# Optimization experiments

Hardware: AMD Instinct MI355X
Metric: run time of the kernel (lower is better)

Reference implementation:

```python
import jax, jax.numpy as jnp
import numpy as np

B, G, D, H, W = 2, 8, 32, 128, 160
NEIGH = 9           # evaluate_neighbors
PROP = 1            # propagation_out_range - 1
PAD1 = int(np.sqrt(NEIGH) / 2) + PROP      # = 2
PAD2 = PAD1 * 2                            # = 4


def setup_inputs() -> dict:
    key = jax.random.key(0)
    ks = jax.random.split(key, 8)
    x1 = jax.random.normal(ks[0], (B, G, D, H, W), jnp.float32)
    offset = jax.random.uniform(ks[1], (B, 2 * NEIGH, H, W), jnp.float32)
    weight = jax.random.uniform(ks[2], (B, 1, H, W), jnp.float32)
    # 1x1x1 Conv3d weights stored as [out_ch, in_ch]; BN folded to scale/bias (eval mode)
    w0 = jax.random.normal(ks[3], (16, G), jnp.float32) * 0.1
    bn0_scale = jnp.ones((16,), jnp.float32)
    bn0_bias = jnp.zeros((16,), jnp.float32)
    w1 = jax.random.normal(ks[4], (8, 16), jnp.float32) * 0.1
    bn1_scale = jnp.ones((8,), jnp.float32)
    bn1_bias = jnp.zeros((8,), jnp.float32)
    w_sim = jax.random.normal(ks[5], (1, 8), jnp.float32) * 0.1
    b_sim = jnp.zeros((1,), jnp.float32)
    return {"x1": x1, "offset": offset, "weight": weight,
            "w0": w0, "bn0_scale": bn0_scale, "bn0_bias": bn0_bias,
            "w1": w1, "bn1_scale": bn1_scale, "bn1_bias": bn1_bias,
            "w_sim": w_sim, "b_sim": b_sim}


def _conv1x1_bn_relu(x, w, scale, bias):
    # x: [B,Cin,D,H,W], w: [Cout,Cin]
    y = jnp.einsum('bcdhw,oc->bodhw', x, w)
    return jax.nn.relu(y * scale[None, :, None, None, None] + bias[None, :, None, None, None])


def reference(x1, offset, weight, w0, bn0_scale, bn0_bias, w1, bn1_scale, bn1_bias, w_sim, b_sim):
    h = _conv1x1_bn_relu(x1, w0, bn0_scale, bn0_bias)          # [B,16,D,H,W]
    h = _conv1x1_bn_relu(h, w1, bn1_scale, bn1_bias)            # [B,8,D,H,W]
    sim = jnp.einsum('bcdhw,oc->bodhw', h, w_sim) + b_sim[None, :, None, None, None]
    sim = sim[:, 0]                                             # [B,D,H,W]
    b, d, hgt, wid = sim.shape
    p1 = jnp.pad(sim, ((0, 0), (0, 0), (PAD1, PAD1), (PAD1, PAD1)), mode='reflect')
    p2 = jnp.pad(sim, ((0, 0), (0, 0), (PAD2, PAD2), (PAD2, PAD2)), mode='reflect')
    side = int(np.sqrt(NEIGH))  # 3
    acc = jnp.zeros_like(sim)
    for s in range(NEIGH):
        iy, ix = s // side, s % side
        # wide-dilation crop (stride (PROP+1)*2 = 4) over the double-padded map
        c2 = p2[:, :, iy * 4: iy * 4 + hgt, ix * 4: ix * 4 + wid]
        # narrow-dilation crop (stride PROP+1 = 2) over the single-padded map
        c1 = p1[:, :, iy * 2: iy * 2 + hgt, ix * 2: ix * 2 + wid]
        w_wide = offset[:, s][:, None]            # [B,1,H,W] -> broadcast over depth
        w_narrow = offset[:, s + NEIGH][:, None]
        acc = acc + (w_narrow * c1 + w_wide * c2) * 0.5
    return acc * weight                                          # weight [B,1,H,W]
```

## Files before the change

### kernel.cpp

```cpp
#include <hip/hip_runtime.h>

#define Bc 2
#define Gc 8
#define Dc 32
#define Hc 128
#define Wc 160
#define HW (Hc * Wc)
#define DHW (Dc * HW)

#define TH 32
#define TW 40
#define R  4
#define SH (TH + 2 * R)
#define SW (TW + 2 * R)
#define SIMN (SH * SW)
#define NQ (SIMN / 4)
#define QPR (SW / 4)
#define NQ2 (TH * TW / 4)
#define QPR2 (TW / 4)

__global__ __launch_bounds__(512)
void fused_kernel(
    const float* __restrict__ x1, const float* __restrict__ offset,
    const float* __restrict__ weight,
    const float* __restrict__ w0, const float* __restrict__ s0, const float* __restrict__ b0,
    const float* __restrict__ w1, const float* __restrict__ s1, const float* __restrict__ b1,
    const float* __restrict__ wsim, const float* __restrict__ bsim,
    float* __restrict__ out)
{
    __shared__ __align__(16) float sms[SIMN];
    __shared__ float smw[289];
    const int tid = threadIdx.x;

    if (tid < 289) {
        const int i = tid;
        float v;
        if (i < 128)      v = w0[i] * s0[i >> 3];
        else if (i < 144) v = b0[i - 128];
        else if (i < 272) v = w1[i - 144] * s1[(i - 144) >> 4];
        else if (i < 280) v = b1[i - 272];
        else if (i < 288) v = wsim[i - 280];
        else              v = bsim[0];
        smw[i] = v;
    }

    const int blk = blockIdx.x;
    const int d   = blk & 31;
    const int t   = (blk >> 5) & 15;
    const int b   = blk >> 9;
    const int h0t = (t >> 2) * TH;
    const int w0t = (t & 3) * TW;

    __syncthreads();

    const float* sw0 = smw;
    const float* sb0 = smw + 128;
    const float* sw1 = smw + 144;
    const float* sb1 = smw + 272;
    const float* sws = smw + 280;
    const float  sbs = smw[288];

    const float* xb = x1 + (size_t)b * (Gc * DHW) + (size_t)d * HW;

    if (tid < NQ) {
        const int q   = tid;
        const int ty  = q / QPR;
        const int tx0 = (q - ty * QPR) * 4;
        int gh = h0t - R + ty;
        gh = gh < 0 ? -gh : (gh >= Hc ? 2 * Hc - 2 - gh : gh);
        const int gw0 = w0t - R + tx0;

        float4 xv[Gc];
        if (gw0 >= 0 && gw0 <= Wc - 4) {
            const float* p = xb + gh * Wc + gw0;
#pragma unroll
            for (int g = 0; g < Gc; ++g)
                xv[g] = *reinterpret_cast<const float4*>(p + g * DHW);
        } else {
            int gw[4];
#pragma unroll
            for (int j = 0; j < 4; ++j) {
                int x = gw0 + j;
                gw[j] = x < 0 ? -x : (x >= Wc ? 2 * Wc - 2 - x : x);
            }
            const float* p = xb + gh * Wc;
#pragma unroll
            for (int g = 0; g < Gc; ++g) {
                xv[g].x = p[g * DHW + gw[0]];
                xv[g].y = p[g * DHW + gw[1]];
                xv[g].z = p[g * DHW + gw[2]];
                xv[g].w = p[g * DHW + gw[3]];
            }
        }

        float4 acc1[8];
#pragma unroll
        for (int c = 0; c < 8; ++c) {
            const float bb = sb1[c];
            acc1[c].x = bb; acc1[c].y = bb; acc1[c].z = bb; acc1[c].w = bb;
        }

#pragma unroll
        for (int o = 0; o < 16; ++o) {
            float ax = sb0[o], ay = ax, az = ax, aw = ax;
#pragma unroll
            for (int g = 0; g < Gc; ++g) {
                const float wv = sw0[o * Gc + g];
                ax = fmaf(wv, xv[g].x, ax);
                ay = fmaf(wv, xv[g].y, ay);
                az = fmaf(wv, xv[g].z, az);
                aw = fmaf(wv, xv[g].w, aw);
            }
            ax = fmaxf(ax, 0.f);
            ay = fmaxf(ay, 0.f);
            az = fmaxf(az, 0.f);
            aw = fmaxf(aw, 0.f);
#pragma unroll
            for (int c = 0; c < 8; ++c) {
                const float wv = sw1[c * 16 + o];
                acc1[c].x = fmaf(wv, ax, acc1[c].x);
                acc1[c].y = fmaf(wv, ay, acc1[c].y);
                acc1[c].z = fmaf(wv, az, acc1[c].z);
                acc1[c].w = fmaf(wv, aw, acc1[c].w);
            }
        }

        float sx = sbs, sy = sbs, sz = sbs, sw = sbs;
#pragma unroll
        for (int c = 0; c < 8; ++c) {
            const float ws = sws[c];
            sx = fmaf(ws, fmaxf(acc1[c].x, 0.f), sx);
            sy = fmaf(ws, fmaxf(acc1[c].y, 0.f), sy);
            sz = fmaf(ws, fmaxf(acc1[c].z, 0.f), sz);
            sw = fmaf(ws, fmaxf(acc1[c].w, 0.f), sw);
        }

        float4 r; r.x = sx; r.y = sy; r.z = sz; r.w = sw;
        *reinterpret_cast<float4*>(&sms[q * 4]) = r;
    }

    __builtin_amdgcn_sched_barrier(0);

    const int oy  = tid / QPR2;
    const int ox  = (tid - oy * QPR2) * 4;
    const int hw4 = (h0t + oy) * Wc + (w0t + ox);

    float4 off4[18];
    float4 wt4;
    if (tid < NQ2) {
        const float* offb = offset + (size_t)b * 18 * HW;
#pragma unroll
        for (int s = 0; s < 18; ++s)
            off4[s] = *reinterpret_cast<const float4*>(offb + s * HW + hw4);
        wt4 = *reinterpret_cast<const float4*>(weight + (size_t)b * HW + hw4);
    }

    __syncthreads();

    if (tid < NQ2) {
        const float* sp = sms + (oy + R) * SW + (ox + R);
        float ax = 0.f, ay = 0.f, az = 0.f, aw = 0.f;
#pragma unroll
        for (int s = 0; s < 9; ++s) {
            const int dy = s / 3 - 1, dx = s % 3 - 1;
            const float4 cw = *reinterpret_cast<const float4*>(sp + dy * 4 * SW + dx * 4);
            const float* np = sp + dy * 2 * SW + dx * 2;
            const float2 n0 = *reinterpret_cast<const float2*>(np);
            const float2 n1 = *reinterpret_cast<const float2*>(np + 2);
            const float4 ow = off4[s];
            const float4 on = off4[s + 9];
            ax = fmaf(on.x, n0.x, fmaf(ow.x, cw.x, ax));
            ay = fmaf(on.y, n0.y, fmaf(ow.y, cw.y, ay));
            az = fmaf(on.z, n1.x, fmaf(ow.z, cw.z, az));
            aw = fmaf(on.w, n1.y, fmaf(ow.w, cw.w, aw));
        }
        float4 r;
        r.x = ax * 0.5f * wt4.x;
        r.y = ay * 0.5f * wt4.y;
        r.z = az * 0.5f * wt4.z;
        r.w = aw * 0.5f * wt4.w;
        float* outb = out + (size_t)(b * Dc + d) * HW;
        *reinterpret_cast<float4*>(outb + hw4) = r;
    }
}

extern "C" void kernel_launch(void* const* d_in, const int* in_sizes, int n_in,
                              void* d_out, int out_size, void* d_ws, size_t ws_size,
                              hipStream_t stream)
{
    const float* x1     = (const float*)d_in[0];
    const float* offset = (const float*)d_in[1];
    const float* weight = (const float*)d_in[2];
    const float* w0     = (const float*)d_in[3];
    const float* s0     = (const float*)d_in[4];
    const float* b0     = (const float*)d_in[5];
    const float* w1     = (const float*)d_in[6];
    const float* s1     = (const float*)d_in[7];
    const float* b1     = (const float*)d_in[8];
    const float* wsim   = (const float*)d_in[9];
    const float* bsim   = (const float*)d_in[10];
    float* out = (float*)d_out;

    fused_kernel<<<1024, 512, 0, stream>>>(x1, offset, weight,
                                           w0, s0, b0, w1, s1, b1, wsim, bsim,
                                           out);
}
```

Measured before the change: 120.0 us.

## Split fused kernel into separate MLP and aggregation kernels via workspace

Replaces the single tiled kernel, which recomputed the per-pixel MLP on halo regions in shared memory, with two kernels. The first computes the similarity map for every voxel once and writes it to the workspace. The second reads neighbors from global memory with reflect indexing and applies the offset-weighted aggregation. This removes redundant halo MLP work and idle threads, at the cost of an extra global round trip for the similarity map and a second launch.

```diff
diff --git a/kernel.cpp b/kernel.cpp
--- a/kernel.cpp
+++ b/kernel.cpp
@@ -8,32 +8,16 @@
 #define HW (Hc * Wc)
 #define DHW (Dc * HW)
 
-#define TH 32
-#define TW 40
-#define R  4
-#define SH (TH + 2 * R)
-#define SW (TW + 2 * R)
-#define SIMN (SH * SW)
-#define NQ (SIMN / 4)
-#define QPR (SW / 4)
-#define NQ2 (TH * TW / 4)
-#define QPR2 (TW / 4)
-
-__global__ __launch_bounds__(512)
-void fused_kernel(
-    const float* __restrict__ x1, const float* __restrict__ offset,
-    const float* __restrict__ weight,
+__global__ __launch_bounds__(256) void mlp_kernel(
+    const float* __restrict__ x1,
     const float* __restrict__ w0, const float* __restrict__ s0, const float* __restrict__ b0,
     const float* __restrict__ w1, const float* __restrict__ s1, const float* __restrict__ b1,
     const float* __restrict__ wsim, const float* __restrict__ bsim,
-    float* __restrict__ out)
+    float* __restrict__ sim)
 {
-    __shared__ __align__(16) float sms[SIMN];
     __shared__ float smw[289];
     const int tid = threadIdx.x;
-
-    if (tid < 289) {
-        const int i = tid;
+    for (int i = tid; i < 289; i += 256) {
         float v;
         if (i < 128)      v = w0[i] * s0[i >> 3];
         else if (i < 144) v = b0[i - 128];
@@ -43,16 +27,7 @@
         else              v = bsim[0];
         smw[i] = v;
     }
-
-    const int blk = blockIdx.x;
-    const int d   = blk & 31;
-    const int t   = (blk >> 5) & 15;
-    const int b   = blk >> 9;
-    const int h0t = (t >> 2) * TH;
-    const int w0t = (t & 3) * TW;
-
     __syncthreads();
-
     const float* sw0 = smw;
     const float* sb0 = smw + 128;
     const float* sw1 = smw + 144;
@@ -60,111 +35,102 @@
     const float* sws = smw + 280;
     const float  sbs = smw[288];
 
-    const float* xb = x1 + (size_t)b * (Gc * DHW) + (size_t)d * HW;
+    const int t   = blockIdx.x * 256 + tid;
+    const int p   = t << 2;
+    const int b   = p / DHW;
+    const int dhw = p - b * DHW;
+    const float* xb = x1 + (size_t)b * (Gc * DHW) + dhw;
 
-    if (tid < NQ) {
-        const int q   = tid;
-        const int ty  = q / QPR;
-        const int tx0 = (q - ty * QPR) * 4;
-        int gh = h0t - R + ty;
-        gh = gh < 0 ? -gh : (gh >= Hc ? 2 * Hc - 2 - gh : gh);
-        const int gw0 = w0t - R + tx0;
+    float4 xv[Gc];
+#pragma unroll
+    for (int g = 0; g < Gc; ++g)
+        xv[g] = *reinterpret_cast<const float4*>(xb + g * DHW);
 
-        float4 xv[Gc];
-        if (gw0 >= 0 && gw0 <= Wc - 4) {
-            const float* p = xb + gh * Wc + gw0;
+    float4 acc1[8];
 #pragma unroll
-            for (int g = 0; g < Gc; ++g)
-                xv[g] = *reinterpret_cast<const float4*>(p + g * DHW);
-        } else {
-            int gw[4];
+    for (int c = 0; c < 8; ++c) {
+        const float bb = sb1[c];
+        acc1[c].x = bb; acc1[c].y = bb; acc1[c].z = bb; acc1[c].w = bb;
+    }
+
 #pragma unroll
-            for (int j = 0; j < 4; ++j) {
-                int x = gw0 + j;
-                gw[j] = x < 0 ? -x : (x >= Wc ? 2 * Wc - 2 - x : x);
-            }
-            const float* p = xb + gh * Wc;
+    for (int o = 0; o < 16; ++o) {
+        float ax = sb0[o], ay = ax, az = ax, aw = ax;
 #pragma unroll
-            for (int g = 0; g < Gc; ++g) {
-                xv[g].x = p[g * DHW + gw[0]];
-                xv[g].y = p[g * DHW + gw[1]];
-                xv[g].z = p[g * DHW + gw[2]];
-                xv[g].w = p[g * DHW + gw[3]];
-            }
+        for (int g = 0; g < Gc; ++g) {
+            const float wv = sw0[o * Gc + g];
+            ax = fmaf(wv, xv[g].x, ax);
+            ay = fmaf(wv, xv[g].y, ay);
+            az = fmaf(wv, xv[g].z, az);
+            aw = fmaf(wv, xv[g].w, aw);
         }
-
-        float4 acc1[8];
+        ax = fmaxf(ax, 0.f);
+        ay = fmaxf(ay, 0.f);
+        az = fmaxf(az, 0.f);
+        aw = fmaxf(aw, 0.f);
 #pragma unroll
         for (int c = 0; c < 8; ++c) {
-            const float bb = sb1[c];
-            acc1[c].x = bb; acc1[c].y = bb; acc1[c].z = bb; acc1[c].w = bb;
+            const float wv = sw1[c * 16 + o];
+            acc1[c].x = fmaf(wv, ax, acc1[c].x);
+            acc1[c].y = fmaf(wv, ay, acc1[c].y);
+            acc1[c].z = fmaf(wv, az, acc1[c].z);
+            acc1[c].w = fmaf(wv, aw, acc1[c].w);
         }
-
-#pragma unroll
-        for (int o = 0; o < 16; ++o) {
-            float ax = sb0[o], ay = ax, az = ax, aw = ax;
-#pragma unroll
-            for (int g = 0; g < Gc; ++g) {
-                const float wv = sw0[o * Gc + g];
-                ax = fmaf(wv, xv[g].x, ax);
-                ay = fmaf(wv, xv[g].y, ay);
-                az = fmaf(wv, xv[g].z, az);
-                aw = fmaf(wv, xv[g].w, aw);
-            }
-            ax = fmaxf(ax, 0.f);
-            ay = fmaxf(ay, 0.f);
-            az = fmaxf(az, 0.f);
-            aw = fmaxf(aw, 0.f);
-#pragma unroll
-            for (int c = 0; c < 8; ++c) {
-                const float wv = sw1[c * 16 + o];
-                acc1[c].x = fmaf(wv, ax, acc1[c].x);
-                acc1[c].y = fmaf(wv, ay, acc1[c].y);
-                acc1[c].z = fmaf(wv, az, acc1[c].z);
-                acc1[c].w = fmaf(wv, aw, acc1[c].w);
-            }
-        }
-
-        float sx = sbs, sy = sbs, sz = sbs, sw = sbs;
-#pragma unroll
-        for (int c = 0; c < 8; ++c) {
-            const float ws = sws[c];
-            sx = fmaf(ws, fmaxf(acc1[c].x, 0.f), sx);
-            sy = fmaf(ws, fmaxf(acc1[c].y, 0.f), sy);
-            sz = fmaf(ws, fmaxf(acc1[c].z, 0.f), sz);
-            sw = fmaf(ws, fmaxf(acc1[c].w, 0.f), sw);
-        }
-
-        float4 r; r.x = sx; r.y = sy; r.z = sz; r.w = sw;
-        *reinterpret_cast<float4*>(&sms[q * 4]) = r;
     }
 
-    __builtin_amdgcn_sched_barrier(0);
-
-    const int oy  = tid / QPR2;
-    const int ox  = (tid - oy * QPR2) * 4;
-    const int hw4 = (h0t + oy) * Wc + (w0t + ox);
-
-    float4 off4[18];
-    float4 wt4;
-    if (tid < NQ2) {
-        const float* offb = offset + (size_t)b * 18 * HW;
+    float sx = sbs, sy = sbs, sz = sbs, sw = sbs;
 #pragma unroll
-        for (int s = 0; s < 18; ++s)
-            off4[s] = *reinterpret_cast<const float4*>(offb + s * HW + hw4);
-        wt4 = *reinterpret_cast<const float4*>(weight + (size_t)b * HW + hw4);
+    for (int c = 0; c < 8; ++c) {
+        const float ws = sws[c];
+        sx = fmaf(ws, fmaxf(acc1[c].x, 0.f), sx);
+        sy = fmaf(ws, fmaxf(acc1[c].y, 0.f), sy);
+        sz = fmaf(ws, fmaxf(acc1[c].z, 0.f), sz);
+        sw = fmaf(ws, fmaxf(acc1[c].w, 0.f), sw);
     }
 
-    __syncthreads();
+    float4 r; r.x = sx; r.y = sy; r.z = sz; r.w = sw;
+    *reinterpret_cast<float4*>(sim + p) = r;
+}
 
-    if (tid < NQ2) {
-        const float* sp = sms + (oy + R) * SW + (ox + R);
-        float ax = 0.f, ay = 0.f, az = 0.f, aw = 0.f;
+__global__ __launch_bounds__(256) void agg_kernel(
+    const float* __restrict__ sim, const float* __restrict__ offset,
+    const float* __restrict__ weight, float* __restrict__ out)
+{
+    const int l  = blockIdx.x * 256 + threadIdx.x;
+    const int q  = l % (Wc / 4);
+    const int w4 = q * 4;
+    int r = l / (Wc / 4);
+    const int h = r % Hc;
+    r /= Hc;
+    const int d = r & 31;
+    const int b = r >> 5;
+    const int hw4 = h * Wc + w4;
+
+    const float* offb = offset + (size_t)b * 18 * HW;
+    float4 off4[18];
+#pragma unroll
+    for (int s = 0; s < 18; ++s)
+        off4[s] = *reinterpret_cast<const float4*>(offb + s * HW + hw4);
+    float4 wt4 = *reinterpret_cast<const float4*>(weight + (size_t)b * HW + hw4);
+    wt4.x *= 0.5f; wt4.y *= 0.5f; wt4.z *= 0.5f; wt4.w *= 0.5f;
+
+    int y1[3], y2[3];
+#pragma unroll
+    for (int iy = 0; iy < 3; ++iy) {
+        int a1 = h + (iy - 1) * 2; y1[iy] = a1 < 0 ? -a1 : (a1 >= Hc ? 2 * Hc - 2 - a1 : a1);
+        int a2 = h + (iy - 1) * 4; y2[iy] = a2 < 0 ? -a2 : (a2 >= Hc ? 2 * Hc - 2 - a2 : a2);
+    }
+
+    const float* sp = sim + (size_t)(b * Dc + d) * HW;
+    float ax = 0.f, ay = 0.f, az = 0.f, aw = 0.f;
+
+    if (w4 >= 4 && w4 <= Wc - 8) {
 #pragma unroll
         for (int s = 0; s < 9; ++s) {
-            const int dy = s / 3 - 1, dx = s % 3 - 1;
-            const float4 cw = *reinterpret_cast<const float4*>(sp + dy * 4 * SW + dx * 4);
-            const float* np = sp + dy * 2 * SW + dx * 2;
+            const int iy = s / 3, ix = s % 3;
+            const float4 cw = *reinterpret_cast<const float4*>(
+                sp + y2[iy] * Wc + w4 + (ix - 1) * 4);
+            const float* np = sp + y1[iy] * Wc + w4 + (ix - 1) * 2;
             const float2 n0 = *reinterpret_cast<const float2*>(np);
             const float2 n1 = *reinterpret_cast<const float2*>(np + 2);
             const float4 ow = off4[s];
@@ -174,14 +140,33 @@
             az = fmaf(on.z, n1.x, fmaf(ow.z, cw.z, az));
             aw = fmaf(on.w, n1.y, fmaf(ow.w, cw.w, aw));
         }
-        float4 r;
-        r.x = ax * 0.5f * wt4.x;
-        r.y = ay * 0.5f * wt4.y;
-        r.z = az * 0.5f * wt4.z;
-        r.w = aw * 0.5f * wt4.w;
-        float* outb = out + (size_t)(b * Dc + d) * HW;
-        *reinterpret_cast<float4*>(outb + hw4) = r;
+    } else {
+        float acc[4] = {0.f, 0.f, 0.f, 0.f};
+#pragma unroll
+        for (int j = 0; j < 4; ++j) {
+            const int w = w4 + j;
+            float a = 0.f;
+#pragma unroll
+            for (int s = 0; s < 9; ++s) {
+                const int iy = s / 3, ix = s % 3;
+                int x1c = w + (ix - 1) * 2; x1c = x1c < 0 ? -x1c : (x1c >= Wc ? 2 * Wc - 2 - x1c : x1c);
+                int x2c = w + (ix - 1) * 4; x2c = x2c < 0 ? -x2c : (x2c >= Wc ? 2 * Wc - 2 - x2c : x2c);
+                const float on = j == 0 ? off4[s + 9].x : j == 1 ? off4[s + 9].y : j == 2 ? off4[s + 9].z : off4[s + 9].w;
+                const float ow = j == 0 ? off4[s].x     : j == 1 ? off4[s].y     : j == 2 ? off4[s].z     : off4[s].w;
+                a = fmaf(on, sp[y1[iy] * Wc + x1c], fmaf(ow, sp[y2[iy] * Wc + x2c], a));
+            }
+            acc[j] = a;
+        }
+        ax = acc[0]; ay = acc[1]; az = acc[2]; aw = acc[3];
     }
+
+    float4 o4;
+    o4.x = ax * wt4.x;
+    o4.y = ay * wt4.y;
+    o4.z = az * wt4.z;
+    o4.w = aw * wt4.w;
+    float* outb = out + (size_t)(b * Dc + d) * HW;
+    *reinterpret_cast<float4*>(outb + hw4) = o4;
 }
 
 extern "C" void kernel_launch(void* const* d_in, const int* in_sizes, int n_in,
@@ -200,8 +185,8 @@
     const float* wsim   = (const float*)d_in[9];
     const float* bsim   = (const float*)d_in[10];
     float* out = (float*)d_out;
+    float* sim = (float*)d_ws;
 
-    fused_kernel<<<1024, 512, 0, stream>>>(x1, offset, weight,
-                                           w0, s0, b0, w1, s1, b1, wsim, bsim,
-                                           out);
+    mlp_kernel<<<1280, 256, 0, stream>>>(x1, w0, s0, b0, w1, s1, b1, wsim, bsim, sim);
+    agg_kernel<<<1280, 256, 0, stream>>>(sim, offset, weight, out);
 }
```

Result: faster. 115.4 us (-3.9%).
